# Kernel optimization log

Hardware: AMD Instinct MI355X
Metric: run time of the kernel (lower is better)

## Reference

```python
import jax, jax.numpy as jnp
import numpy as np

BN_EPS = 1e-5

# Binary_a: sign forward, hard-tanh STE backward (grad zeroed where |x| >= 1)
@jax.custom_vjp
def binary_act(x):
    return jnp.sign(x)

def _ba_fwd(x):
    return jnp.sign(x), x

def _ba_bwd(x, g):
    return (jnp.where((x > -1.0) & (x < 1.0), g, 0.0),)

binary_act.defvjp(_ba_fwd, _ba_bwd)

# Binary_w: sign forward, identity STE backward
@jax.custom_vjp
def binary_w(x):
    return jnp.sign(x)

def _bw_fwd(x):
    return jnp.sign(x), None

def _bw_bwd(_, g):
    return (g,)

binary_w.defvjp(_bw_fwd, _bw_bwd)


def setup_inputs() -> dict:
    key = jax.random.key(0)
    k1, k2, k3 = jax.random.split(key, 3)
    B, Cin, Cout, H, Wd, K = 32, 256, 256, 56, 56, 3
    x = jax.random.normal(k1, (B, Cin, H, Wd), dtype=jnp.float32)
    weight = jax.random.normal(k2, (Cout, Cin, K, K), dtype=jnp.float32) * 0.05
    bias = jax.random.normal(k3, (Cout,), dtype=jnp.float32) * 0.01
    gamma = jnp.ones((Cout,), dtype=jnp.float32)
    beta = jnp.zeros((Cout,), dtype=jnp.float32)
    return {"x": x, "weight": weight, "bias": bias, "gamma": gamma, "beta": beta}


def reference(x, weight, bias, gamma, beta):
    # activation binarization (A=2)
    xb = binary_act(x)
    # weight quantization (W=2): mean-center over in-channel dim, clamp to [-1,1]
    # (done on .data in torch -> values change but no grad through this step)
    wc_val = jnp.clip(weight - jnp.mean(weight, axis=1, keepdims=True), -1.0, 1.0)
    wc = weight + jax.lax.stop_gradient(wc_val - weight)
    # per-output-filter scale alpha = E[|w|] over (in, kh, kw)
    alpha = jnp.mean(jnp.abs(wc), axis=(1, 2, 3), keepdims=True)
    wq = binary_w(wc) * alpha  # [O,I,K,K]
    # conv2d, stride 1, padding 1, groups 1
    y = jax.lax.conv_general_dilated(
        xb, wq, window_strides=(1, 1), padding=((1, 1), (1, 1)),
        dimension_numbers=("NCHW", "OIHW", "NCHW"))
    y = y + bias[None, :, None, None]
    # BatchNorm2d, training-mode forward (biased batch stats)
    mean = jnp.mean(y, axis=(0, 2, 3), keepdims=True)
    var = jnp.mean(jnp.square(y - mean), axis=(0, 2, 3), keepdims=True)
    y = (y - mean) * jax.lax.rsqrt(var + BN_EPS)
    y = y * gamma[None, :, None, None] + beta[None, :, None, None]
    # last_relu=1
    return jax.nn.relu(y)
```

## Files before the change

kernel.cpp:

```cpp
#include <hip/hip_runtime.h>
#include <stdint.h>

typedef unsigned long long u64;
typedef unsigned int u32;
typedef int v4i __attribute__((ext_vector_type(4)));
typedef int v16i __attribute__((ext_vector_type(16)));

#define B_    32
#define CIN   256
#define COUT  256
#define H_    56
#define W_    56
#define HW    3136
#define NPOS  100352
#define NROW  1792
#define NPACKBLK 784


__global__ __launch_bounds__(256) void k_prep(
    const float* __restrict__ x,
    const float* __restrict__ wgt,
    u64* __restrict__ xbits,
    int8_t* __restrict__ Bfrag,
    float* __restrict__ alpha,
    int* __restrict__ ssum,
    unsigned long long* __restrict__ qsum)
{
    const int tid = threadIdx.x;

    if (blockIdx.x < NPACKBLK) {
        const int j = blockIdx.x / 196;
        const int p2 = (blockIdx.x - j * 196) * 256 + tid;
        const int pos0 = p2 * 2;
        const int b = pos0 / HW;
        const int hw = pos0 - b * HW;
        const float* xp = x + (size_t)b * CIN * HW + (size_t)j * 64 * HW + hw;
        u64 b0 = 0, b1 = 0;
#pragma unroll 8
        for (int k = 0; k < 64; ++k) {
            const float2 v = *(const float2*)(xp + (size_t)k * HW);
            b0 |= (u64)(v.x > 0.0f) << k;
            b1 |= (u64)(v.y > 0.0f) << k;
        }
        xbits[(size_t)pos0 * 4 + j] = b0;
        xbits[(size_t)(pos0 + 1) * 4 + j] = b1;
        return;
    }

    const int o = blockIdx.x - NPACKBLK;
    const int i = tid;
    const int wave = i >> 6, lane = i & 63;
    __shared__ float sred[4][12];

    if (i == 0) { ssum[o] = 0; qsum[o] = 0ULL; }

    float w9[9];
#pragma unroll
    for (int t = 0; t < 9; ++t) w9[t] = wgt[(o * 256 + i) * 9 + t];

    float m[9];
#pragma unroll
    for (int t = 0; t < 9; ++t) m[t] = w9[t];
#pragma unroll
    for (int s = 1; s < 64; s <<= 1)
#pragma unroll
        for (int t = 0; t < 9; ++t) m[t] += __shfl_xor(m[t], s, 64);
    if (lane == 0) {
#pragma unroll
        for (int t = 0; t < 9; ++t) sred[wave][t] = m[t];
    }
    __syncthreads();
#pragma unroll
    for (int t = 0; t < 9; ++t)
        m[t] = (sred[0][t] + sred[1][t] + sred[2][t] + sred[3][t]) * (1.0f / 256.0f);

    float wc[9];
    float asum = 0.0f;
#pragma unroll
    for (int t = 0; t < 9; ++t) {
        float v = w9[t] - m[t];
        v = fminf(fmaxf(v, -1.0f), 1.0f);
        wc[t] = v;
        asum += fabsf(v);
    }
#pragma unroll
    for (int s = 1; s < 64; s <<= 1) asum += __shfl_xor(asum, s, 64);
    __syncthreads();
    if (lane == 0) sred[wave][9] = asum;
    __syncthreads();
    if (i == 0)
        alpha[o] = (sred[0][9] + sred[1][9] + sred[2][9] + sred[3][9]) * (1.0f / 2304.0f);

#pragma unroll
    for (int t = 0; t < 9; ++t) {
        const int8_t sv = (wc[t] > 0.0f) ? (int8_t)1 : (int8_t)-1;
        const size_t addr =
            ((size_t)((t * 8 + (i >> 5)) * 8 + (o >> 5)) * 64
             + (size_t)(((i >> 4) & 1) * 32 + (o & 31))) * 16 + (i & 15);
        Bfrag[addr] = sv;
    }
}

#define MFMA_I8(acc, a, b) \
    asm volatile("v_mfma_i32_32x32x32_i8 %0, %1, %2, %0" : "+a"(acc) : "v"(a), "v"(b))

__global__ __launch_bounds__(256, 3) void kc_mfma(
    const u64* __restrict__ xbits,
    const int8_t* __restrict__ Bfrag,
    short* __restrict__ S,
    int* __restrict__ ssum,
    unsigned long long* __restrict__ qsum)
{
    const int blk = blockIdx.x;
    const int b = blk / H_;
    const int h = blk - b * H_;
    const int tid = threadIdx.x;

    __shared__ u32 ldsb[3 * 58 * 64];

    for (int it = tid; it < 3 * 58 * 16; it += 256) {
        const int r = it / 928;
        const int rem = it - r * 928;
        const int wp = rem >> 4;
        const int g = rem & 15;
        const int hr = h - 1 + r;
        const int w_in = wp - 1;
        const bool inb = (hr >= 0) && (hr < H_) && (w_in >= 0) && (w_in < W_);
        u32 chunk16 = 0;
        if (inb) {
            const u64 word = xbits[((size_t)(b * HW + hr * W_ + w_in)) * 4 + (g >> 2)];
            chunk16 = (u32)(word >> ((g & 3) * 16)) & 0xFFFFu;
        }
        u32 out4[4];
#pragma unroll
        for (int d = 0; d < 4; ++d) {
            const u32 nib = (chunk16 >> (4 * d)) & 0xFu;
            const u32 m1 = (nib * 0x00204081u) & 0x01010101u;
            const u32 inv = m1 ^ 0x01010101u;
            out4[d] = inb ? (0x01010101u ^ (inv * 0xFEu)) : 0u;
        }
        const int gs = (g + wp) & 15;
        u32* dst = &ldsb[((r * 58 + wp) << 6) + gs * 4];
        dst[0] = out4[0]; dst[1] = out4[1]; dst[2] = out4[2]; dst[3] = out4[3];
    }
    __syncthreads();

    const int m0 = tid & 31;
    const int lh = (tid >> 5) & 1;
    const int wv = tid >> 6;
    const int8_t* smem = (const int8_t*)ldsb;
    const int8_t* Bp = Bfrag + (size_t)(tid & 63) * 16;

    auto ldA = [&](int kk, int mt) -> v4i {
        const int tap = kk >> 3, s = kk & 7;
        const int dh = tap / 3;
        const int dw = tap - dh * 3;
        const int wpm = min(mt * 32 + m0 + dw, 57);
        const int gs = (2 * s + lh + wpm) & 15;
        const int addr = ((dh * 58 + wpm) << 8) + (gs << 4);
        return *(const v4i*)(smem + addr);
    };
    auto ldB = [&](int kk, int ntl) -> v4i {
        const size_t off = (size_t)((kk * 8) + wv * 2 + ntl) * 1024;
        return *(const v4i*)(Bp + off);
    };

    v16i acc00 = {0}, acc01 = {0}, acc10 = {0}, acc11 = {0};
    v4i A0[2], A1[2], Bb0[2], Bb1[2];

    A0[0] = ldA(0, 0); A1[0] = ldA(0, 1);
    Bb0[0] = ldB(0, 0); Bb1[0] = ldB(0, 1);

#pragma unroll
    for (int kk = 0; kk < 72; ++kk) {
        const int cur = kk & 1, nxt = cur ^ 1;
        if (kk < 71) {
            A0[nxt] = ldA(kk + 1, 0); A1[nxt] = ldA(kk + 1, 1);
            Bb0[nxt] = ldB(kk + 1, 0); Bb1[nxt] = ldB(kk + 1, 1);
        }
        MFMA_I8(acc00, A0[cur], Bb0[cur]);
        MFMA_I8(acc01, A0[cur], Bb1[cur]);
        MFMA_I8(acc10, A1[cur], Bb0[cur]);
        MFMA_I8(acc11, A1[cur], Bb1[cur]);
    }

    asm volatile("s_nop 7\n\ts_nop 7\n\ts_nop 7"
                 : "+a"(acc00), "+a"(acc01), "+a"(acc10), "+a"(acc11));

    const int n0 = wv * 64 + m0;
    const int n1 = n0 + 32;
    const int rowbase = b * HW + h * W_;
    int s0 = 0, s1 = 0, q0 = 0, q1 = 0;

#pragma unroll
    for (int reg = 0; reg < 16; ++reg) {
        const int m = (reg & 3) + ((reg >> 2) << 3) + (lh << 2);
        const int v0 = acc00[reg], v1 = acc01[reg];
        s0 += v0; q0 += v0 * v0; s1 += v1; q1 += v1 * v1;
        S[(size_t)(rowbase + m) * 256 + n0] = (short)v0;
        S[(size_t)(rowbase + m) * 256 + n1] = (short)v1;
    }
#pragma unroll
    for (int reg = 0; reg < 12; ++reg) {
        const int m = 32 + (reg & 3) + ((reg >> 2) << 3) + (lh << 2);
        const int v0 = acc10[reg], v1 = acc11[reg];
        s0 += v0; q0 += v0 * v0; s1 += v1; q1 += v1 * v1;
        S[(size_t)(rowbase + m) * 256 + n0] = (short)v0;
        S[(size_t)(rowbase + m) * 256 + n1] = (short)v1;
    }

    s0 += __shfl_xor(s0, 32, 64); q0 += __shfl_xor(q0, 32, 64);
    s1 += __shfl_xor(s1, 32, 64); q1 += __shfl_xor(q1, 32, 64);
    if (lh == 0) {
        atomicAdd(&ssum[n0], s0);
        atomicAdd(&qsum[n0], (unsigned long long)(long long)q0);
        atomicAdd(&ssum[n1], s1);
        atomicAdd(&qsum[n1], (unsigned long long)(long long)q1);
    }
}

__global__ __launch_bounds__(256) void kb_apply(
    const short* __restrict__ S,
    const int* __restrict__ ssum,
    const unsigned long long* __restrict__ qsum,
    const float* __restrict__ alpha,
    const float* __restrict__ gamma,
    const float* __restrict__ beta,
    float* __restrict__ out)
{
    const int blk = blockIdx.x;
    const int chunk = blk % 49;
    const int bcg = blk / 49;
    const int cg = bcg & 3;
    const int b = bcg >> 2;
    const int c0 = cg * 64;
    const int p0 = chunk * 64;
    const int tid = threadIdx.x;

    __shared__ float s_scale[64], s_shift[64];
    __shared__ u32 lds[64 * 33];

    if (tid < 64) {
        const int o = c0 + tid;
        const double N = (double)NPOS;
        double meanS = (double)ssum[o] / N;
        double varS = (double)qsum[o] / N - meanS * meanS;
        double a = (double)alpha[o];
        double rstd = 1.0 / sqrt(a * a * varS + 1e-5);
        double g = (double)gamma[o];
        s_scale[tid] = (float)(g * a * rstd);
        s_shift[tid] = (float)((double)beta[o] - g * a * meanS * rstd);
    }

    const u32* Sp = (const u32*)(S + ((size_t)b * HW + p0) * 256 + c0);
#pragma unroll
    for (int k = 0; k < 8; ++k) {
        const int idx = tid + k * 256;
        const int p = idx >> 5, cp = idx & 31;
        lds[p * 33 + cp] = Sp[p * 128 + cp];
    }
    __syncthreads();

    const int pl = tid & 63;
    const int ch4 = tid >> 6;
    const short* lss = (const short*)lds;
#pragma unroll
    for (int cc = 0; cc < 16; ++cc) {
        const int c = ch4 * 16 + cc;
        const float f = fmaxf(fmaf((float)lss[pl * 66 + c], s_scale[c], s_shift[c]), 0.0f);
        out[((size_t)(b * COUT + c0 + c)) * HW + p0 + pl] = f;
    }
}

extern "C" void kernel_launch(void* const* d_in, const int* in_sizes, int n_in,
                              void* d_out, int out_size, void* d_ws, size_t ws_size,
                              hipStream_t stream) {
    const float* x     = (const float*)d_in[0];
    const float* wgt   = (const float*)d_in[1];
    const float* gamma = (const float*)d_in[3];
    const float* beta  = (const float*)d_in[4];
    float* out = (float*)d_out;

    char* ws = (char*)d_ws;
    int8_t* Bfrag = (int8_t*)(ws + 0);
    float* alpha = (float*)(ws + 589824);
    int*   ssum  = (int*)(ws + 590848);
    unsigned long long* qsum = (unsigned long long*)(ws + 591872);
    u64*   xbits = (u64*)(ws + 593920);
    short* Sarr  = (short*)(ws + 3805184);

    k_prep<<<NPACKBLK + 256, 256, 0, stream>>>(x, wgt, xbits, Bfrag, alpha, ssum, qsum);
    kc_mfma<<<NROW, 256, 0, stream>>>(xbits, Bfrag, Sarr, ssum, qsum);
    kb_apply<<<32 * 4 * 49, 256, 0, stream>>>(Sarr, ssum, qsum, alpha, gamma, beta, out);
}
```

Before: 277.6 us.

## Compute two output rows per block in binary conv MFMA kernel

Each block of the int8 MFMA convolution kernel now handles two output rows instead of one. It stages four input rows in LDS and doubles the M tiles per wave, from two to four. Each B-fragment load is now reused across twice as many MFMAs, and the overlapping input halo is staged once per pair of rows rather than once per row. In exchange the accumulators double, occupancy drops to two blocks per SM, and only half as many blocks are launched.

After: 283.3 us. +2.0%, slower.

```diff
diff --git a/kernel.cpp b/kernel.cpp
--- a/kernel.cpp
+++ b/kernel.cpp
@@ -104,7 +104,7 @@
 #define MFMA_I8(acc, a, b) \
     asm volatile("v_mfma_i32_32x32x32_i8 %0, %1, %2, %0" : "+a"(acc) : "v"(a), "v"(b))
 
-__global__ __launch_bounds__(256, 3) void kc_mfma(
+__global__ __launch_bounds__(256, 2) void kc_mfma(
     const u64* __restrict__ xbits,
     const int8_t* __restrict__ Bfrag,
     short* __restrict__ S,
@@ -112,23 +112,24 @@
     unsigned long long* __restrict__ qsum)
 {
     const int blk = blockIdx.x;
-    const int b = blk / H_;
-    const int h = blk - b * H_;
+    const int b = blk / 28;
+    const int hp = blk - b * 28;
+    const int h0 = hp * 2;
     const int tid = threadIdx.x;
 
-    __shared__ u32 ldsb[3 * 58 * 64];
-
-    for (int it = tid; it < 3 * 58 * 16; it += 256) {
+    __shared__ u32 ldsb[4 * 58 * 64];
+
+    for (int it = tid; it < 4 * 58 * 16; it += 256) {
         const int r = it / 928;
         const int rem = it - r * 928;
         const int wp = rem >> 4;
         const int g = rem & 15;
-        const int hr = h - 1 + r;
+        const int ir = h0 - 1 + r;
         const int w_in = wp - 1;
-        const bool inb = (hr >= 0) && (hr < H_) && (w_in >= 0) && (w_in < W_);
+        const bool inb = (ir >= 0) && (ir < H_) && (w_in >= 0) && (w_in < W_);
         u32 chunk16 = 0;
         if (inb) {
-            const u64 word = xbits[((size_t)(b * HW + hr * W_ + w_in)) * 4 + (g >> 2)];
+            const u64 word = xbits[((size_t)(b * HW + ir * W_ + w_in)) * 4 + (g >> 2)];
             chunk16 = (u32)(word >> ((g & 3) * 16)) & 0xFFFFu;
         }
         u32 out4[4];
@@ -155,9 +156,10 @@
         const int tap = kk >> 3, s = kk & 7;
         const int dh = tap / 3;
         const int dw = tap - dh * 3;
-        const int wpm = min(mt * 32 + m0 + dw, 57);
+        const int r = dh + (mt >> 1);
+        const int wpm = min((mt & 1) * 32 + m0 + dw, 57);
         const int gs = (2 * s + lh + wpm) & 15;
-        const int addr = ((dh * 58 + wpm) << 8) + (gs << 4);
+        const int addr = ((r * 58 + wpm) << 8) + (gs << 4);
         return *(const v4i*)(smem + addr);
     };
     auto ldB = [&](int kk, int ntl) -> v4i {
@@ -165,48 +167,55 @@
         return *(const v4i*)(Bp + off);
     };
 
-    v16i acc00 = {0}, acc01 = {0}, acc10 = {0}, acc11 = {0};
-    v4i A0[2], A1[2], Bb0[2], Bb1[2];
-
-    A0[0] = ldA(0, 0); A1[0] = ldA(0, 1);
-    Bb0[0] = ldB(0, 0); Bb1[0] = ldB(0, 1);
+    v16i acc[4][2];
+#pragma unroll
+    for (int mt = 0; mt < 4; ++mt)
+#pragma unroll
+        for (int ntl = 0; ntl < 2; ++ntl) acc[mt][ntl] = (v16i){0};
+
+    v4i A[2][4], Bb[2][2];
+#pragma unroll
+    for (int mt = 0; mt < 4; ++mt) A[0][mt] = ldA(0, mt);
+    Bb[0][0] = ldB(0, 0); Bb[0][1] = ldB(0, 1);
 
 #pragma unroll
     for (int kk = 0; kk < 72; ++kk) {
         const int cur = kk & 1, nxt = cur ^ 1;
         if (kk < 71) {
-            A0[nxt] = ldA(kk + 1, 0); A1[nxt] = ldA(kk + 1, 1);
-            Bb0[nxt] = ldB(kk + 1, 0); Bb1[nxt] = ldB(kk + 1, 1);
-        }
-        MFMA_I8(acc00, A0[cur], Bb0[cur]);
-        MFMA_I8(acc01, A0[cur], Bb1[cur]);
-        MFMA_I8(acc10, A1[cur], Bb0[cur]);
-        MFMA_I8(acc11, A1[cur], Bb1[cur]);
-    }
-
-    asm volatile("s_nop 7\n\ts_nop 7\n\ts_nop 7"
-                 : "+a"(acc00), "+a"(acc01), "+a"(acc10), "+a"(acc11));
+#pragma unroll
+            for (int mt = 0; mt < 4; ++mt) A[nxt][mt] = ldA(kk + 1, mt);
+            Bb[nxt][0] = ldB(kk + 1, 0); Bb[nxt][1] = ldB(kk + 1, 1);
+        }
+#pragma unroll
+        for (int mt = 0; mt < 4; ++mt) {
+            MFMA_I8(acc[mt][0], A[cur][mt], Bb[cur][0]);
+            MFMA_I8(acc[mt][1], A[cur][mt], Bb[cur][1]);
+        }
+    }
+
+#pragma unroll
+    for (int mt = 0; mt < 4; ++mt)
+        asm volatile("s_nop 7\n\ts_nop 7" : "+a"(acc[mt][0]), "+a"(acc[mt][1]));
 
     const int n0 = wv * 64 + m0;
     const int n1 = n0 + 32;
-    const int rowbase = b * HW + h * W_;
     int s0 = 0, s1 = 0, q0 = 0, q1 = 0;
 
 #pragma unroll
-    for (int reg = 0; reg < 16; ++reg) {
-        const int m = (reg & 3) + ((reg >> 2) << 3) + (lh << 2);
-        const int v0 = acc00[reg], v1 = acc01[reg];
-        s0 += v0; q0 += v0 * v0; s1 += v1; q1 += v1 * v1;
-        S[(size_t)(rowbase + m) * 256 + n0] = (short)v0;
-        S[(size_t)(rowbase + m) * 256 + n1] = (short)v1;
-    }
-#pragma unroll
-    for (int reg = 0; reg < 12; ++reg) {
-        const int m = 32 + (reg & 3) + ((reg >> 2) << 3) + (lh << 2);
-        const int v0 = acc10[reg], v1 = acc11[reg];
-        s0 += v0; q0 += v0 * v0; s1 += v1; q1 += v1 * v1;
-        S[(size_t)(rowbase + m) * 256 + n0] = (short)v0;
-        S[(size_t)(rowbase + m) * 256 + n1] = (short)v1;
+    for (int mt = 0; mt < 4; ++mt) {
+        const int nreg = (mt & 1) ? 12 : 16;
+        const int rowb = b * HW + (h0 + (mt >> 1)) * W_;
+        const int mb = (mt & 1) * 32;
+#pragma unroll
+        for (int reg = 0; reg < 16; ++reg) {
+            if (reg < nreg) {
+                const int m = mb + (reg & 3) + ((reg >> 2) << 3) + (lh << 2);
+                const int v0 = acc[mt][0][reg], v1 = acc[mt][1][reg];
+                s0 += v0; q0 += v0 * v0; s1 += v1; q1 += v1 * v1;
+                S[(size_t)(rowb + m) * 256 + n0] = (short)v0;
+                S[(size_t)(rowb + m) * 256 + n1] = (short)v1;
+            }
+        }
     }
 
     s0 += __shfl_xor(s0, 32, 64); q0 += __shfl_xor(q0, 32, 64);
@@ -290,6 +299,6 @@
     short* Sarr  = (short*)(ws + 3805184);
 
     k_prep<<<NPACKBLK + 256, 256, 0, stream>>>(x, wgt, xbits, Bfrag, alpha, ssum, qsum);
-    kc_mfma<<<NROW, 256, 0, stream>>>(xbits, Bfrag, Sarr, ssum, qsum);
+    kc_mfma<<<32 * 28, 256, 0, stream>>>(xbits, Bfrag, Sarr, ssum, qsum);
     kb_apply<<<32 * 4 * 49, 256, 0, stream>>>(Sarr, ssum, qsum, alpha, gamma, beta, out);
 }
```
